# Kernel tuning notes

Hardware: AMD Instinct MI355X
Metric: run time of the kernel (lower is better)

Reference implementation:

```python
import jax, jax.numpy as jnp
import numpy as np

DIM = 512; D_STATE = 8; D_CONV = 3; EXPAND = 1; WIN = 7; N = WIN * WIN
D_INNER = EXPAND * DIM; D_HALF = D_INNER // 2
DT_RANK = -(-DIM // 16)  # 32
E = DT_RANK + 2 * D_STATE  # 48
B_WIN = 512


def _diag_flat(w):
    idx = []
    for s in range(2 * w - 1):
        for r in range(max(0, s - (w - 1)), min(w - 1, s) + 1):
            idx.append(r * w + (s - r))
    return np.array(idx, dtype=np.int32)


def _anti_flat(w):
    idx = []
    for s in range(2 * w - 1):
        for r in range(max(0, s - (w - 1)), min(w - 1, s) + 1):
            c = s - r
            idx.append(r * w + (w - 1 - c))
    return np.array(idx, dtype=np.int32)

DIAG_IDX = jnp.asarray(_diag_flat(WIN))
ANTI_IDX = jnp.asarray(_anti_flat(WIN))
V_IDX = jnp.asarray(np.arange(N).reshape(WIN, WIN).T.reshape(-1).astype(np.int32))


def setup_inputs() -> dict:
    key = jax.random.key(0)
    ks = iter(jax.random.split(key, 32))
    f32 = jnp.float32
    def lin_w(k, out_d, in_d):
        return (jax.random.normal(k, (out_d, in_d), f32) * (in_d ** -0.5)).astype(f32)
    inp = {}
    inp['tokens'] = jax.random.normal(next(ks), (B_WIN, N, DIM), f32)
    for nm in ['pre_h', 'pre_v', 'pre_d', 'pre_a', 'post_h', 'post_v', 'post_d', 'post_a']:
        inp[nm + '_w'] = lin_w(next(ks), DIM, DIM)
        inp[nm + '_b'] = jnp.zeros((DIM,), f32)
    inp['in_proj_w'] = lin_w(next(ks), D_INNER, DIM)
    inp['conv_x_w'] = jax.random.normal(next(ks), (D_HALF, 1, D_CONV), f32) * (D_CONV ** -0.5)
    inp['conv_x_b'] = jnp.zeros((D_HALF,), f32)
    inp['conv_z_w'] = jax.random.normal(next(ks), (D_HALF, 1, D_CONV), f32) * (D_CONV ** -0.5)
    inp['conv_z_b'] = jnp.zeros((D_HALF,), f32)
    inp['x_proj_w'] = lin_w(next(ks), E, D_HALF)
    inp['ln_w'] = jnp.ones((E,), f32)
    inp['ln_b'] = jnp.zeros((E,), f32)
    dt_std = DT_RANK ** -0.5
    inp['dt_proj_w'] = jax.random.uniform(next(ks), (D_HALF, DT_RANK), f32, -dt_std, dt_std)
    u = jax.random.uniform(next(ks), (D_HALF,), f32)
    dt = jnp.clip(jnp.exp(u * (np.log(0.1) - np.log(0.001)) + np.log(0.001)), 1e-4, None)
    inp['dt_proj_b'] = dt + jnp.log(-jnp.expm1(-dt))
    inp['A_log'] = jnp.tile(jnp.log(jnp.arange(1, D_STATE + 1, dtype=f32))[None, :], (D_HALF, 1))
    inp['D_param'] = jnp.ones((D_HALF,), f32)
    inp['out_proj_w'] = lin_w(next(ks), DIM, D_INNER)
    inp['gate_logits'] = jnp.zeros((4,), f32)
    return inp


def _linear(x, W, b=None):
    y = x @ W.T
    return y if b is None else y + b


def _dwconv_same(x, w, b):
    # x: (b, d, l), w: (d, 1, k) depthwise, cross-correlation like torch
    y = jax.lax.conv_general_dilated(x, w, window_strides=(1,), padding='SAME',
                                     dimension_numbers=('NCH', 'OIH', 'NCH'),
                                     feature_group_count=x.shape[1])
    return y + b[None, :, None]


def _layernorm(x, g, b, eps=1e-5):
    m = jnp.mean(x, -1, keepdims=True)
    v = jnp.var(x, -1, keepdims=True)
    return (x - m) * jax.lax.rsqrt(v + eps) * g + b


def _selective_scan(u, delta, A, Bm, Cm, D, delta_bias):
    # u, delta: (b,d,l); A: (d,n); Bm, Cm: (b,n,l); D: (d,)
    delta = jax.nn.softplus(delta + delta_bias[None, :, None])
    u_l = jnp.moveaxis(u, 2, 0)       # (l,b,d)
    d_l = jnp.moveaxis(delta, 2, 0)   # (l,b,d)
    B_l = jnp.moveaxis(Bm, 2, 0)      # (l,b,n)
    C_l = jnp.moveaxis(Cm, 2, 0)      # (l,b,n)
    h0 = jnp.zeros((u.shape[0], u.shape[1], A.shape[1]), u.dtype)  # (b,d,n)

    def step(h, t):
        dt_t, u_t, B_t, C_t = t
        dA = jnp.exp(dt_t[:, :, None] * A[None])          # (b,d,n)
        dBu = dt_t[:, :, None] * B_t[:, None, :] * u_t[:, :, None]
        h = h * dA + dBu
        y = jnp.einsum('bdn,bn->bd', h, C_t)
        return h, y

    _, ys = jax.lax.scan(step, h0, (d_l, u_l, B_l, C_l))
    y = jnp.moveaxis(ys, 0, 2)  # (b,d,l)
    return y + D[None, :, None] * u


def _mamba_core(x_seq, p):
    b, L, _ = x_seq.shape
    xz = _linear(x_seq, p['in_proj_w'])              # (b,l,d_inner)
    xz = jnp.swapaxes(xz, 1, 2)                      # (b,d_inner,l)
    x, z = jnp.split(xz, 2, axis=1)                  # each (b,d_half,l)
    x_conv = jax.nn.silu(_dwconv_same(x, p['conv_x_w'], p['conv_x_b']))
    z_conv = jax.nn.silu(_dwconv_same(z, p['conv_z_w'], p['conv_z_b']))
    A = -jnp.exp(p['A_log'])
    x_dbl = jnp.einsum('bdl,ed->ble', x_conv, p['x_proj_w'])  # (b,l,E)
    x_dbl = _layernorm(x_dbl, p['ln_w'], p['ln_b'])
    dt, Bm, Cm = jnp.split(x_dbl, [DT_RANK, DT_RANK + D_STATE], axis=-1)
    dt = jnp.swapaxes(_linear(dt, p['dt_proj_w']), 1, 2)      # (b,d_half,l)
    Bm = jnp.swapaxes(Bm, 1, 2)                                # (b,n,l)
    Cm = jnp.swapaxes(Cm, 1, 2)
    y = _selective_scan(x_conv, dt, A, Bm, Cm, p['D_param'], p['dt_proj_b'])
    y = jnp.nan_to_num(y)
    y = jnp.concatenate([y, z_conv], axis=1)                   # (b,d_inner,l)
    y = jnp.swapaxes(y, 1, 2)
    return _linear(y, p['out_proj_w'])


def reference(tokens, pre_h_w, pre_h_b, pre_v_w, pre_v_b, pre_d_w, pre_d_b,
              pre_a_w, pre_a_b, in_proj_w, conv_x_w, conv_x_b, conv_z_w, conv_z_b,
              x_proj_w, ln_w, ln_b, dt_proj_w, dt_proj_b, A_log, D_param,
              out_proj_w, post_h_w, post_h_b, post_v_w, post_v_b, post_d_w,
              post_d_b, post_a_w, post_a_b, gate_logits):
    p = dict(in_proj_w=in_proj_w, conv_x_w=conv_x_w, conv_x_b=conv_x_b,
             conv_z_w=conv_z_w, conv_z_b=conv_z_b, x_proj_w=x_proj_w,
             ln_w=ln_w, ln_b=ln_b, dt_proj_w=dt_proj_w, dt_proj_b=dt_proj_b,
             A_log=A_log, D_param=D_param, out_proj_w=out_proj_w)
    rh = _linear(tokens, pre_h_w, pre_h_b)
    rv = _linear(tokens, pre_v_w, pre_v_b)[:, V_IDX, :]
    rd = _linear(tokens, pre_d_w, pre_d_b)[:, DIAG_IDX, :]
    ra = _linear(tokens, pre_a_w, pre_a_b)[:, ANTI_IDX, :]
    r_all = jnp.concatenate([rh, rv, rd, ra], axis=0)
    y_all = _mamba_core(r_all, p)
    yh, yv, yd, ya = jnp.split(y_all, 4, axis=0)
    yh = _linear(yh, post_h_w, post_h_b)
    yv = _linear(yv, post_v_w, post_v_b)
    yd = _linear(yd, post_d_w, post_d_b)
    ya = _linear(ya, post_a_w, post_a_b)
    g = jax.nn.softmax(gate_logits)
    return g[0] * yh + g[1] * yv + g[2] * yd + g[3] * ya
```

## Files before the change

kernel.cpp:

```cpp
#include <hip/hip_runtime.h>
#include <stdint.h>

typedef __attribute__((ext_vector_type(8))) short bf16x8;
typedef __attribute__((ext_vector_type(4))) float f32x4;

__device__ __forceinline__ float bf2f(short u){
  union { float f; uint32_t i; } v; v.i = ((uint32_t)(uint16_t)u) << 16; return v.f;
}
__device__ __forceinline__ short f2bf(float x){
  union { float f; uint32_t i; } v; v.f = x;
  uint32_t r = v.i + 0x7FFFu + ((v.i >> 16) & 1u);
  return (short)(r >> 16);
}

__device__ __forceinline__ void gl_lds16(const short* g, short* l){
  __builtin_amdgcn_global_load_lds(
      (__attribute__((address_space(1))) void*)(short*)g,
      (__attribute__((address_space(3))) void*)l, 16, 0, 0);
}

__device__ const int d_DIAG[49] = {0,1,7,2,8,14,3,9,15,21,4,10,16,22,28,5,11,17,23,29,35,
  6,12,18,24,30,36,42,13,19,25,31,37,43,20,26,32,38,44,27,33,39,45,34,40,46,41,47,48};
__device__ const int d_ANTI[49] = {6,5,13,4,12,20,3,11,19,27,2,10,18,26,34,1,9,17,25,33,41,
  0,8,16,24,32,40,48,7,15,23,31,39,47,14,22,30,38,46,21,29,37,45,28,36,44,35,43,42};

__device__ __forceinline__ int perm_idx(int g, int l){
  if (g == 0) return l;
  if (g == 1) return (l % 7) * 7 + l / 7;
  if (g == 2) return d_DIAG[l];
  return d_ANTI[l];
}

template<int NT>
__device__ __forceinline__ void kcore256x128(
    const short* aU0, const short* aU1, const short* bU,
    short* S, int w, int lane, f32x4 acc[4][4])
{
  int wr = w >> 1, wc = w & 1;
  int mr = lane & 15, quad = lane >> 4;
  int sw = (quad ^ ((mr >> 1) & 3)) * 8;
  auto STAGE_A = [&](int t){
    short* base = S + (t & 1) * 12288;
    gl_lds16(aU0 + t*32, base + (w*32)*32);
    gl_lds16(aU1 + t*32, base + (w*32 + 16)*32);
  };
  auto STAGE_B = [&](int t){
    short* base = S + (t & 1) * 12288;
    gl_lds16(bU + t*32, base + 8192 + (w*16)*32);
  };
  STAGE_A(0); STAGE_B(0);
  if (NT > 1) STAGE_A(1);
  asm volatile("s_waitcnt vmcnt(2)" ::: "memory");
  __builtin_amdgcn_s_barrier();
  for (int t = 0; t < NT; ++t){
    const short* Ab = S + (t & 1) * 12288;
    const short* Bb = Ab + 8192;
    bf16x8 bfr[4];
    #pragma unroll
    for (int nf = 0; nf < 4; ++nf)
      bfr[nf] = *(const bf16x8*)(Bb + (wc*64 + nf*16 + mr)*32 + sw);
    #pragma unroll
    for (int ph = 0; ph < 4; ++ph){
      bf16x8 af = *(const bf16x8*)(Ab + (wr*64 + ph*16 + mr)*32 + sw);
      if (ph == 1 && t+1 < NT) STAGE_B(t+1);
      #pragma unroll
      for (int nf = 0; nf < 4; ++nf)
        acc[ph][nf] = __builtin_amdgcn_mfma_f32_16x16x32_bf16(af, bfr[nf], acc[ph][nf],0,0,0);
    }
    __builtin_amdgcn_s_barrier();
    if (t+2 < NT){
      STAGE_A(t+2);
      asm volatile("s_waitcnt vmcnt(2)" ::: "memory");
    } else if (t+1 < NT){
      asm volatile("s_waitcnt vmcnt(0)" ::: "memory");
    }
    __builtin_amdgcn_s_barrier();
  }
}

__global__ __launch_bounds__(256) void k_conv_all(
    const float* __restrict__ in_proj,
    const float* __restrict__ pw0, const float* __restrict__ pw1,
    const float* __restrict__ pw2, const float* __restrict__ pw3,
    const float* __restrict__ xpw, const float* __restrict__ dtw,
    short* __restrict__ inp_bf, short* __restrict__ postw_bf,
    short* __restrict__ xpw_bf, short* __restrict__ dtw_bf)
{
  int q = blockIdx.x*256 + threadIdx.x;
  const float* src; short* dst; int off;
  if (q < 65536){ src = in_proj; dst = inp_bf; off = q; }
  else if (q < 65536 + 262144){
    int r = q - 65536; int g = r >> 16; int loc = r & 65535;
    src = (g==0)?pw0:(g==1)?pw1:(g==2)?pw2:pw3;
    dst = postw_bf + g*262144; off = loc;
  }
  else if (q < 65536 + 262144 + 3072){ src = xpw; dst = xpw_bf; off = q - (65536+262144); }
  else { src = dtw; dst = dtw_bf; off = q - (65536+262144+3072); }
  float4 v = *(const float4*)(src + off*4);
  uint32_t p0 = (uint32_t)(uint16_t)f2bf(v.x) | ((uint32_t)(uint16_t)f2bf(v.y) << 16);
  uint32_t p1 = (uint32_t)(uint16_t)f2bf(v.z) | ((uint32_t)(uint16_t)f2bf(v.w) << 16);
  uint2 p; p.x = p0; p.y = p1;
  *(uint2*)(dst + off*4) = p;
}

__global__ __launch_bounds__(256) void k_transp(
    const float* __restrict__ pw0, const float* __restrict__ pw1,
    const float* __restrict__ pw2, const float* __restrict__ pw3,
    const float* __restrict__ outp,
    short* __restrict__ wpreT, short* __restrict__ woutT)
{
  __shared__ float tile[64][65];
  int which = blockIdx.y;
  const float* src = (which==0)?pw0:(which==1)?pw1:(which==2)?pw2:(which==3)?pw3:outp;
  short* dst = (which < 4) ? (wpreT + which*262144) : woutT;
  int bi = blockIdx.x >> 3, bj = blockIdx.x & 7;
  int r0 = bi*64, c0 = bj*64;
  int t = threadIdx.x;
  int row = t >> 2, cg = t & 3;
  const float4* s4 = (const float4*)(src + (r0+row)*512 + c0 + cg*16);
  #pragma unroll
  for (int i=0;i<4;i++){
    float4 v = s4[i];
    tile[row][cg*16 + i*4 + 0] = v.x;
    tile[row][cg*16 + i*4 + 1] = v.y;
    tile[row][cg*16 + i*4 + 2] = v.z;
    tile[row][cg*16 + i*4 + 3] = v.w;
  }
  __syncthreads();
  int oc = t >> 2;
  short tmp[16];
  #pragma unroll
  for (int i=0;i<16;i++) tmp[i] = f2bf(tile[cg*16 + i][oc]);
  short* dp = dst + (size_t)(c0+oc)*512 + r0 + cg*16;
  *(bf16x8*)(dp)     = *(bf16x8*)tmp;
  *(bf16x8*)(dp + 8) = *((bf16x8*)tmp + 1);
}

__global__ __launch_bounds__(256) void k_tok(const float* __restrict__ t, short* __restrict__ o){
  int i = (blockIdx.x*256 + threadIdx.x) * 4;
  float4 v = *(const float4*)(t + i);
  uint32_t p0 = (uint32_t)(uint16_t)f2bf(v.x) | ((uint32_t)(uint16_t)f2bf(v.y) << 16);
  uint32_t p1 = (uint32_t)(uint16_t)f2bf(v.z) | ((uint32_t)(uint16_t)f2bf(v.w) << 16);
  uint2 p; p.x = p0; p.y = p1;
  *(uint2*)(o + i) = p;
}

__global__ __launch_bounds__(256) void k_bxz_gains(const float* __restrict__ in_proj,
    const float* __restrict__ b0, const float* __restrict__ b1,
    const float* __restrict__ b2, const float* __restrict__ b3,
    const float* __restrict__ gl,
    const float* __restrict__ pb0, const float* __restrict__ pb1,
    const float* __restrict__ pb2, const float* __restrict__ pb3,
    float* __restrict__ bxz, float* __restrict__ gains, float* __restrict__ biasc)
{
  if (blockIdx.x < 8){
    int idx = blockIdx.x*256 + threadIdx.x;
    int g = idx >> 9, i = idx & 511;
    const float* bb = (g==0)?b0:(g==1)?b1:(g==2)?b2:b3;
    float s = 0.f;
    for (int t=0;t<512;t++) s += in_proj[i*512+t]*bb[t];
    bxz[idx] = s;
  } else {
    float m = fmaxf(fmaxf(gl[0], gl[1]), fmaxf(gl[2], gl[3]));
    float e0 = expf(gl[0]-m), e1 = expf(gl[1]-m), e2 = expf(gl[2]-m), e3 = expf(gl[3]-m);
    float s = e0+e1+e2+e3;
    float g0 = e0/s, g1 = e1/s, g2 = e2/s, g3 = e3/s;
    int t = threadIdx.x;
    if (t == 0){ gains[0]=g0; gains[1]=g1; gains[2]=g2; gains[3]=g3; }
    biasc[t]     = g0*pb0[t]     + g1*pb1[t]     + g2*pb2[t]     + g3*pb3[t];
    biasc[t+256] = g0*pb0[t+256] + g1*pb1[t+256] + g2*pb2[t+256] + g3*pb3[t+256];
  }
}

__device__ __forceinline__ void mfma_2x4_k(const short* a0, const short* a1,
    const short* b0, const short* b1, const short* b2, const short* b3,
    int K, f32x4 acc[2][4])
{
  for (int k0 = 0; k0 < K; k0 += 32){
    bf16x8 av0 = *(const bf16x8*)(a0 + k0);
    bf16x8 av1 = *(const bf16x8*)(a1 + k0);
    bf16x8 bv0 = *(const bf16x8*)(b0 + k0);
    bf16x8 bv1 = *(const bf16x8*)(b1 + k0);
    bf16x8 bv2 = *(const bf16x8*)(b2 + k0);
    bf16x8 bv3 = *(const bf16x8*)(b3 + k0);
    acc[0][0] = __builtin_amdgcn_mfma_f32_16x16x32_bf16(av0, bv0, acc[0][0],0,0,0);
    acc[0][1] = __builtin_amdgcn_mfma_f32_16x16x32_bf16(av0, bv1, acc[0][1],0,0,0);
    acc[0][2] = __builtin_amdgcn_mfma_f32_16x16x32_bf16(av0, bv2, acc[0][2],0,0,0);
    acc[0][3] = __builtin_amdgcn_mfma_f32_16x16x32_bf16(av0, bv3, acc[0][3],0,0,0);
    acc[1][0] = __builtin_amdgcn_mfma_f32_16x16x32_bf16(av1, bv0, acc[1][0],0,0,0);
    acc[1][1] = __builtin_amdgcn_mfma_f32_16x16x32_bf16(av1, bv1, acc[1][1],0,0,0);
    acc[1][2] = __builtin_amdgcn_mfma_f32_16x16x32_bf16(av1, bv2, acc[1][2],0,0,0);
    acc[1][3] = __builtin_amdgcn_mfma_f32_16x16x32_bf16(av1, bv3, acc[1][3],0,0,0);
  }
}

__global__ __launch_bounds__(256) void k_wfuse(const short* __restrict__ inp_bf,
    const short* __restrict__ wpreT, const short* __restrict__ postw_bf,
    const short* __restrict__ woutT, const float* __restrict__ gains,
    short* __restrict__ wxz, short* __restrict__ wogc)
{
  int z = blockIdx.z; int g = z & 3, which = z >> 2;
  int bn = blockIdx.x * 64, bm = blockIdx.y * 128;
  int lane = threadIdx.x & 63, wave = threadIdx.x >> 6;
  int mr = lane & 15, qk = (lane >> 4) * 8, quad = lane >> 4;
  const short* Am = which ? (postw_bf + g*262144) : inp_bf;
  const short* Bm = which ? woutT : (wpreT + g*262144);
  const short* a0 = Am + (bm + wave*32 + mr)*512 + qk;
  const short* a1 = a0 + 16*512;
  const short* b0 = Bm + (bn +  0 + mr)*512 + qk;
  const short* b1 = Bm + (bn + 16 + mr)*512 + qk;
  const short* b2 = Bm + (bn + 32 + mr)*512 + qk;
  const short* b3 = Bm + (bn + 48 + mr)*512 + qk;
  f32x4 acc[2][4] = {};
  mfma_2x4_k(a0, a1, b0, b1, b2, b3, 512, acc);
  float gain = which ? gains[g] : 1.f;
  #pragma unroll
  for (int s=0;s<2;s++)
    #pragma unroll
    for (int t=0;t<4;t++)
      #pragma unroll
      for (int r=0;r<4;r++){
        int row = bm + wave*32 + s*16 + quad*4 + r;
        int col = bn + t*16 + mr;
        if (which) wogc[row*2048 + g*512 + col] = f2bf(gain * acc[s][t][r]);
        else       wxz[g*262144 + row*512 + col] = f2bf(acc[s][t][r]);
      }
}

__global__ __launch_bounds__(512) void k_gemm1c(const short* __restrict__ tok,
    const short* __restrict__ wxz, const float* __restrict__ bxz,
    const float* __restrict__ cxw, const float* __restrict__ cxb,
    const float* __restrict__ czw, const float* __restrict__ czb,
    short* __restrict__ ycat)
{
  __shared__ __align__(16) short S[24576];
  int bid = blockIdx.x;
  int swz = (bid & 7) * 206 + (bid >> 3);
  int g = swz / 412, rem = swz - g*412;
  int blk = rem >> 2, bn = (rem & 3) * 128;
  int bm = blk * 245;
  int nreal = min(245, 25088 - bm);
  int tid = threadIdx.x, lane = tid & 63, w = tid >> 6;

  int rl = lane >> 2;
  int gch = ((lane & 3) ^ ((lane >> 3) & 3)) * 8;
  const short* aU[2];
  #pragma unroll
  for (int j = 0; j < 2; ++j){
    int p = w*32 + j*16 + rl;
    int pr = (p < nreal) ? p : (nreal - 1);
    int q49 = pr / 49;
    int l49 = pr - q49*49;
    int b = blk*5 + q49;
    int sl = perm_idx(g, l49);
    aU[j] = tok + ((size_t)(b*49 + sl))*512 + gch;
  }
  const short* bU = wxz + (size_t)g*262144 + (size_t)(bn + w*16 + rl)*512 + gch;

  f32x4 acc[4][4] = {};
  kcore256x128<16>(aU[0], aU[1], bU, S, w, lane, acc);

  int wr = w >> 1, wc = w & 1, mr = lane & 15, quad = lane >> 4;
  int rowgrp = tid >> 3, oct = tid & 7;
  #pragma unroll
  for (int h = 0; h < 2; ++h){
    if (wc == h){
      #pragma unroll
      for (int mf = 0; mf < 4; ++mf)
        #pragma unroll
        for (int nf = 0; nf < 4; ++nf)
          #pragma unroll
          for (int rr = 0; rr < 4; ++rr){
            int row = wr*64 + mf*16 + quad*4 + rr;
            int col = nf*16 + mr;
            S[row*72 + col] = f2bf(acc[mf][nf][rr] + bxz[g*512 + bn + h*64 + col]);
          }
    }
    __syncthreads();
    int colbase = bn + h*64 + oct*8;
    bool isx = colbase < 256;
    const float* wsrc = isx ? cxw : czw;
    const float* bsrc = isx ? cxb : czb;
    int cc0 = isx ? colbase : colbase - 256;
    float w0[8], w1[8], w2[8], cb[8];
    #pragma unroll
    for (int e = 0; e < 8; ++e){
      w0[e] = wsrc[(cc0+e)*3]; w1[e] = wsrc[(cc0+e)*3+1]; w2[e] = wsrc[(cc0+e)*3+2];
      cb[e] = bsrc[cc0+e];
    }
    for (int i = 0; i < 4; ++i){
      int p = rowgrp + 64*i;
      if (p < nreal){
        int l = p - (p/49)*49;
        bf16x8 vm = {}, vp = {};
        bf16x8 v0 = *(const bf16x8*)(S + p*72 + oct*8);
        if (l > 0)  vm = *(const bf16x8*)(S + (p-1)*72 + oct*8);
        if (l < 48) vp = *(const bf16x8*)(S + (p+1)*72 + oct*8);
        short ov[8];
        #pragma unroll
        for (int e = 0; e < 8; ++e){
          float x = w0[e]*bf2f(vm[e]) + w1[e]*bf2f(v0[e]) + w2[e]*bf2f(vp[e]) + cb[e];
          ov[e] = f2bf(x / (1.f + __expf(-x)));
        }
        *(bf16x8*)(ycat + (size_t)(bm + p)*2048 + g*512 + colbase) = *(bf16x8*)ov;
      }
    }
    __syncthreads();
  }
}

__global__ __launch_bounds__(256) void k_xproj(const short* __restrict__ ycat,
    const short* __restrict__ xpw_bf, const float* __restrict__ lnw, const float* __restrict__ lnb,
    const short* __restrict__ dtw_bf, const float* __restrict__ dtb,
    short* __restrict__ dtln, float* __restrict__ bc)
{
  __shared__ __align__(16) char smem[36864];
  float* xd = (float*)smem;
  short* xln = (short*)(smem + 26624);

  int bm = blockIdx.x * 128;
  int g = bm / 25088;
  int tid = threadIdx.x, lane = tid & 63, w = tid >> 6;
  int mr = lane & 15, quad = lane >> 4, qk = quad * 8;

  {
    const short* ap[2];
    #pragma unroll
    for (int s=0;s<2;s++)
      ap[s] = ycat + (size_t)(bm - g*25088 + w*32 + s*16 + mr)*2048 + g*512 + qk;
    f32x4 acc[2][3] = {};
    #pragma unroll
    for (int k0 = 0; k0 < 256; k0 += 32){
      bf16x8 av[2];
      #pragma unroll
      for (int s=0;s<2;s++) av[s] = *(const bf16x8*)(ap[s] + k0);
      #pragma unroll
      for (int t=0;t<3;t++){
        bf16x8 bv = *(const bf16x8*)(xpw_bf + (t*16 + mr)*256 + qk + k0);
        #pragma unroll
        for (int s=0;s<2;s++)
          acc[s][t] = __builtin_amdgcn_mfma_f32_16x16x32_bf16(av[s], bv, acc[s][t],0,0,0);
      }
    }
    #pragma unroll
    for (int s=0;s<2;s++)
      #pragma unroll
      for (int t=0;t<3;t++)
        #pragma unroll
        for (int r=0;r<4;r++)
          xd[(w*32 + s*16 + quad*4 + r)*52 + t*16 + mr] = acc[s][t][r];
  }
  __syncthreads();

  if (tid < 128){
    f32x4* xr4 = (f32x4*)(xd + tid*52);
    f32x4 s = xr4[0];
    #pragma unroll
    for (int i=1;i<12;i++) s += xr4[i];
    float m = (s[0]+s[1]+s[2]+s[3]) * (1.f/48.f);
    f32x4 vs = {};
    #pragma unroll
    for (int i=0;i<12;i++){ f32x4 d = xr4[i] - m; vs += d*d; }
    float var = (vs[0]+vs[1]+vs[2]+vs[3]) * (1.f/48.f);
    float rstd = rsqrtf(var + 1e-5f);
    const f32x4* g4 = (const f32x4*)lnw;
    const f32x4* b4 = (const f32x4*)lnb;
    uint32_t* xlr = (uint32_t*)(xln + tid*40);
    #pragma unroll
    for (int i=0;i<8;i++){
      f32x4 v = (xr4[i] - m) * rstd * g4[i] + b4[i];
      xlr[2*i]   = (uint32_t)(uint16_t)f2bf(v[0]) | ((uint32_t)(uint16_t)f2bf(v[1]) << 16);
      xlr[2*i+1] = (uint32_t)(uint16_t)f2bf(v[2]) | ((uint32_t)(uint16_t)f2bf(v[3]) << 16);
    }
    f32x4* bco = (f32x4*)(bc + (size_t)(bm + tid)*16);
    #pragma unroll
    for (int i=8;i<12;i++)
      bco[i-8] = (xr4[i] - m) * rstd * g4[i] + b4[i];
  }
  __syncthreads();

  {
    bf16x8 a[2];
    #pragma unroll
    for (int s=0;s<2;s++)
      a[s] = *(const bf16x8*)(xln + (w*32 + s*16 + mr)*40 + qk);
    #pragma unroll 4
    for (int nt=0; nt<16; nt++){
      int col = nt*16 + mr;
      bf16x8 bv = *(const bf16x8*)(dtw_bf + col*32 + qk);
      float dtbv = dtb[col];
      #pragma unroll
      for (int s=0;s<2;s++){
        f32x4 acc = {};
        acc = __builtin_amdgcn_mfma_f32_16x16x32_bf16(a[s], bv, acc,0,0,0);
        #pragma unroll
        for (int r=0;r<4;r++){
          int grow = bm + w*32 + s*16 + quad*4 + r;
          float dtv = acc[r] + dtbv;
          float e  = __expf(dtv);
          float sp = __logf(1.f + e);
          float delta = (dtv > 15.f) ? dtv : sp;
          dtln[(size_t)grow*256 + col] = f2bf(delta);
        }
      }
    }
  }
}

__global__ __launch_bounds__(256) void k_scan(short* __restrict__ ycat,
    const short* __restrict__ dtln, const float* __restrict__ bc,
    const float* __restrict__ Alog, const float* __restrict__ Dp)
{
  __shared__ __align__(16) float bcs[784];
  int gb = blockIdx.x; int g = gb >> 9, b = gb & 511;
  int d = threadIdx.x;
  if (d < 196) ((f32x4*)bcs)[d] = ((const f32x4*)(bc + (size_t)gb*784))[d];
  __syncthreads();

  float A[8], h[8];
  {
    f32x4 a0 = *(const f32x4*)(Alog + d*8);
    f32x4 a1 = *(const f32x4*)(Alog + d*8 + 4);
    #pragma unroll
    for (int n=0;n<4;n++){ A[n] = -__expf(a0[n]); A[n+4] = -__expf(a1[n]); h[n]=0.f; h[n+4]=0.f; }
  }
  float Dpar = Dp[d];

  const short* dptr = dtln + (size_t)gb*49*256 + d;
  short* uptr = ycat + (size_t)(b*49)*2048 + g*512 + d;

  float dn = bf2f(dptr[0]);
  float un = bf2f(uptr[0]);
  for (int l=0;l<49;l++){
    float delta = dn, u = un;
    if (l < 48){ dn = bf2f(dptr[(l+1)*256]); un = bf2f(uptr[(l+1)*2048]); }
    const f32x4* bcr = (const f32x4*)(bcs + l*16);
    f32x4 B0 = bcr[0], B1 = bcr[1], C0 = bcr[2], C1 = bcr[3];
    float du = delta * u;
    float y = 0.f;
    #pragma unroll
    for (int n=0;n<4;n++){
      h[n] = h[n]*__expf(delta*A[n]) + du*B0[n];
      y += h[n]*C0[n];
    }
    #pragma unroll
    for (int n=0;n<4;n++){
      h[n+4] = h[n+4]*__expf(delta*A[n+4]) + du*B1[n];
      y += h[n+4]*C1[n];
    }
    uptr[l*2048] = f2bf(y + Dpar*u);
  }
}

__global__ __launch_bounds__(512) void k_gemmF(const short* __restrict__ ycat,
    const short* __restrict__ wogc, const float* __restrict__ biasc,
    float* __restrict__ out)
{
  __shared__ __align__(16) short S[24576];
  int bid = blockIdx.x;
  int swz = (bid & 7) * 49 + (bid >> 3);
  int bm = (swz >> 2) * 256, bn = (swz & 3) * 128;
  int tid = threadIdx.x, lane = tid & 63, w = tid >> 6;

  int rl = lane >> 2;
  int gch = ((lane & 3) ^ ((lane >> 3) & 3)) * 8;
  const short* aU0 = ycat + (size_t)(bm + w*32      + rl)*2048 + gch;
  const short* aU1 = ycat + (size_t)(bm + w*32 + 16 + rl)*2048 + gch;
  const short* bU  = wogc + (size_t)(bn + w*16      + rl)*2048 + gch;

  f32x4 acc[4][4] = {};
  kcore256x128<64>(aU0, aU1, bU, S, w, lane, acc);

  int wr = w >> 1, wc = w & 1, mr = lane & 15, quad = lane >> 4;
  #pragma unroll
  for (int mf = 0; mf < 4; ++mf)
    #pragma unroll
    for (int rr = 0; rr < 4; ++rr){
      int row = bm + wr*64 + mf*16 + quad*4 + rr;
      float* orow = out + (size_t)row*512;
      #pragma unroll
      for (int nf = 0; nf < 4; ++nf){
        int col = bn + wc*64 + nf*16 + mr;
        orow[col] = acc[mf][nf][rr] + biasc[col];
      }
    }
}

extern "C" void kernel_launch(void* const* d_in, const int* in_sizes, int n_in,
                              void* d_out, int out_size, void* d_ws, size_t ws_size,
                              hipStream_t stream)
{
  const float* tokens    = (const float*)d_in[0];
  const float* pre_w[4]  = {(const float*)d_in[1], (const float*)d_in[3], (const float*)d_in[5], (const float*)d_in[7]};
  const float* pre_b[4]  = {(const float*)d_in[2], (const float*)d_in[4], (const float*)d_in[6], (const float*)d_in[8]};
  const float* post_w[4] = {(const float*)d_in[9], (const float*)d_in[11], (const float*)d_in[13], (const float*)d_in[15]};
  const float* post_b[4] = {(const float*)d_in[10], (const float*)d_in[12], (const float*)d_in[14], (const float*)d_in[16]};
  const float* in_proj   = (const float*)d_in[17];
  const float* conv_x_w  = (const float*)d_in[18];
  const float* conv_x_b  = (const float*)d_in[19];
  const float* conv_z_w  = (const float*)d_in[20];
  const float* conv_z_b  = (const float*)d_in[21];
  const float* x_proj_w  = (const float*)d_in[22];
  const float* ln_w      = (const float*)d_in[23];
  const float* ln_b      = (const float*)d_in[24];
  const float* dt_proj_w = (const float*)d_in[25];
  const float* dt_proj_b = (const float*)d_in[26];
  const float* A_log     = (const float*)d_in[27];
  const float* D_param   = (const float*)d_in[28];
  const float* out_proj  = (const float*)d_in[29];
  const float* gate_log  = (const float*)d_in[30];

  char* ws = (char*)d_ws;
  size_t o = 0;
  short* tok_bf   = (short*)(ws + o); o += 25690112;
  short* wpreT    = (short*)(ws + o); o += 2097152;
  short* inp_bf   = (short*)(ws + o); o += 524288;
  short* postw_bf = (short*)(ws + o); o += 2097152;
  short* woutT    = (short*)(ws + o); o += 524288;
  short* wogc     = (short*)(ws + o); o += 2097152;
  short* wxz      = (short*)(ws + o); o += 2097152;
  short* xpw_bf   = (short*)(ws + o); o += 24576;
  short* dtw_bf   = (short*)(ws + o); o += 16384;
  float* bxz      = (float*)(ws + o); o += 8192;
  float* gains    = (float*)(ws + o); o += 64;
  float* biasc    = (float*)(ws + o); o += 2048;
  size_t scratch_off = o;
  o += 102760448;
  short* ycat     = (short*)(ws + o); o += 102760448;
  short* dtln     = (short*)(ws + scratch_off);
  float* bc       = (float*)(ws + scratch_off + 51380224);

  k_conv_all<<<1300, 256, 0, stream>>>(in_proj,
      post_w[0], post_w[1], post_w[2], post_w[3],
      x_proj_w, dt_proj_w, inp_bf, postw_bf, xpw_bf, dtw_bf);
  k_transp<<<dim3(64,5), 256, 0, stream>>>(pre_w[0], pre_w[1], pre_w[2], pre_w[3],
      out_proj, wpreT, woutT);
  k_tok<<<12544, 256, 0, stream>>>(tokens, tok_bf);
  k_bxz_gains<<<9, 256, 0, stream>>>(in_proj, pre_b[0], pre_b[1], pre_b[2], pre_b[3],
      gate_log, post_b[0], post_b[1], post_b[2], post_b[3], bxz, gains, biasc);
  k_wfuse<<<dim3(8,4,8), 256, 0, stream>>>(inp_bf, wpreT, postw_bf, woutT, gains, wxz, wogc);
  k_gemm1c<<<dim3(1648), 512, 0, stream>>>(tok_bf, wxz, bxz,
      conv_x_w, conv_x_b, conv_z_w, conv_z_b, ycat);
  k_xproj<<<784, 256, 0, stream>>>(ycat, xpw_bf, ln_w, ln_b, dtw_bf, dt_proj_b, dtln, bc);
  k_scan<<<2048, 256, 0, stream>>>(ycat, dtln, bc, A_log, D_param);
  k_gemmF<<<dim3(392), 512, 0, stream>>>(ycat, wogc, biasc, (float*)d_out);
}
```

Baseline: 453.1 us.

## Fuse x-projection, layernorm, dt projection and selective scan into one kernel

Merges the x_proj/LN/dt_proj kernel with the selective scan kernel so each block handles one (group, window) sequence of 49 tokens. The u tile, delta and B/C values stay in LDS instead of going through global scratch buffers, which removes the dtln/bc write and read traffic and one kernel launch. In exchange, the MFMA tiles are padded from 49 to 64 rows, which wastes some compute, and the larger LDS footprint of about 58KB per block may reduce occupancy. A block-index swizzle is also added.

```diff
diff --git a/kernel.cpp b/kernel.cpp
--- a/kernel.cpp
+++ b/kernel.cpp
@@ -309,50 +309,55 @@
   }
 }
 
-__global__ __launch_bounds__(256) void k_xproj(const short* __restrict__ ycat,
+__global__ __launch_bounds__(256) void k_xps(short* __restrict__ ycat,
     const short* __restrict__ xpw_bf, const float* __restrict__ lnw, const float* __restrict__ lnb,
     const short* __restrict__ dtw_bf, const float* __restrict__ dtb,
-    short* __restrict__ dtln, float* __restrict__ bc)
-{
-  __shared__ __align__(16) char smem[36864];
-  float* xd = (float*)smem;
-  short* xln = (short*)(smem + 26624);
-
-  int bm = blockIdx.x * 128;
-  int g = bm / 25088;
+    const float* __restrict__ Alog, const float* __restrict__ Dp)
+{
+  __shared__ __align__(16) char smem[58016];
+  short* Us  = (short*)smem;
+  short* xln = (short*)(smem + 25872);
+  float* bcs = (float*)(smem + 29792);
+  float* xd  = (float*)(smem + 32928);
+  short* ddt = (short*)(smem + 32928);
+
+  int bid = blockIdx.x;
+  int swz = (bid & 7) * 256 + (bid >> 3);
+  int g = swz >> 9, b = swz & 511;
   int tid = threadIdx.x, lane = tid & 63, w = tid >> 6;
   int mr = lane & 15, quad = lane >> 4, qk = quad * 8;
 
+  const short* ubase = ycat + (size_t)(b*49)*2048 + g*512;
+  for (int idx = tid; idx < 1568; idx += 256){
+    int l = idx >> 5, cc = (idx & 31) * 8;
+    *(bf16x8*)(Us + l*264 + cc) = *(const bf16x8*)(ubase + (size_t)l*2048 + cc);
+  }
+  __syncthreads();
+
   {
-    const short* ap[2];
-    #pragma unroll
-    for (int s=0;s<2;s++)
-      ap[s] = ycat + (size_t)(bm - g*25088 + w*32 + s*16 + mr)*2048 + g*512 + qk;
-    f32x4 acc[2][3] = {};
+    int ar = w*16 + mr; if (ar > 48) ar = 48;
+    const short* ap = Us + ar*264 + qk;
+    f32x4 acc[3] = {};
     #pragma unroll
     for (int k0 = 0; k0 < 256; k0 += 32){
-      bf16x8 av[2];
-      #pragma unroll
-      for (int s=0;s<2;s++) av[s] = *(const bf16x8*)(ap[s] + k0);
-      #pragma unroll
-      for (int t=0;t<3;t++){
+      bf16x8 av = *(const bf16x8*)(ap + k0);
+      #pragma unroll
+      for (int t = 0; t < 3; ++t){
         bf16x8 bv = *(const bf16x8*)(xpw_bf + (t*16 + mr)*256 + qk + k0);
-        #pragma unroll
-        for (int s=0;s<2;s++)
-          acc[s][t] = __builtin_amdgcn_mfma_f32_16x16x32_bf16(av[s], bv, acc[s][t],0,0,0);
-      }
-    }
-    #pragma unroll
-    for (int s=0;s<2;s++)
-      #pragma unroll
-      for (int t=0;t<3;t++)
-        #pragma unroll
-        for (int r=0;r<4;r++)
-          xd[(w*32 + s*16 + quad*4 + r)*52 + t*16 + mr] = acc[s][t][r];
+        acc[t] = __builtin_amdgcn_mfma_f32_16x16x32_bf16(av, bv, acc[t],0,0,0);
+      }
+    }
+    #pragma unroll
+    for (int t = 0; t < 3; ++t)
+      #pragma unroll
+      for (int r = 0; r < 4; ++r){
+        int row = w*16 + quad*4 + r;
+        if (row < 49) xd[row*52 + t*16 + mr] = acc[t][r];
+      }
   }
   __syncthreads();
 
-  if (tid < 128){
+  if (tid < 49){
     f32x4* xr4 = (f32x4*)(xd + tid*52);
     f32x4 s = xr4[0];
     #pragma unroll
@@ -372,7 +377,7 @@
       xlr[2*i]   = (uint32_t)(uint16_t)f2bf(v[0]) | ((uint32_t)(uint16_t)f2bf(v[1]) << 16);
       xlr[2*i+1] = (uint32_t)(uint16_t)f2bf(v[2]) | ((uint32_t)(uint16_t)f2bf(v[3]) << 16);
     }
-    f32x4* bco = (f32x4*)(bc + (size_t)(bm + tid)*16);
+    f32x4* bco = (f32x4*)(bcs + tid*16);
     #pragma unroll
     for (int i=8;i<12;i++)
       bco[i-8] = (xr4[i] - m) * rstd * g4[i] + b4[i];
@@ -380,75 +385,59 @@
   __syncthreads();
 
   {
-    bf16x8 a[2];
-    #pragma unroll
-    for (int s=0;s<2;s++)
-      a[s] = *(const bf16x8*)(xln + (w*32 + s*16 + mr)*40 + qk);
+    int ar = w*16 + mr; if (ar > 48) ar = 48;
+    bf16x8 a = *(const bf16x8*)(xln + ar*40 + qk);
     #pragma unroll 4
     for (int nt=0; nt<16; nt++){
       int col = nt*16 + mr;
       bf16x8 bv = *(const bf16x8*)(dtw_bf + col*32 + qk);
       float dtbv = dtb[col];
-      #pragma unroll
-      for (int s=0;s<2;s++){
-        f32x4 acc = {};
-        acc = __builtin_amdgcn_mfma_f32_16x16x32_bf16(a[s], bv, acc,0,0,0);
-        #pragma unroll
-        for (int r=0;r<4;r++){
-          int grow = bm + w*32 + s*16 + quad*4 + r;
+      f32x4 acc = {};
+      acc = __builtin_amdgcn_mfma_f32_16x16x32_bf16(a, bv, acc,0,0,0);
+      #pragma unroll
+      for (int r=0;r<4;r++){
+        int row = w*16 + quad*4 + r;
+        if (row < 49){
           float dtv = acc[r] + dtbv;
           float e  = __expf(dtv);
           float sp = __logf(1.f + e);
           float delta = (dtv > 15.f) ? dtv : sp;
-          dtln[(size_t)grow*256 + col] = f2bf(delta);
+          ddt[row*256 + col] = f2bf(delta);
         }
       }
     }
   }
-}
-
-__global__ __launch_bounds__(256) void k_scan(short* __restrict__ ycat,
-    const short* __restrict__ dtln, const float* __restrict__ bc,
-    const float* __restrict__ Alog, const float* __restrict__ Dp)
-{
-  __shared__ __align__(16) float bcs[784];
-  int gb = blockIdx.x; int g = gb >> 9, b = gb & 511;
-  int d = threadIdx.x;
-  if (d < 196) ((f32x4*)bcs)[d] = ((const f32x4*)(bc + (size_t)gb*784))[d];
   __syncthreads();
 
-  float A[8], h[8];
   {
+    int d = tid;
+    float A[8], h[8];
     f32x4 a0 = *(const f32x4*)(Alog + d*8);
     f32x4 a1 = *(const f32x4*)(Alog + d*8 + 4);
     #pragma unroll
     for (int n=0;n<4;n++){ A[n] = -__expf(a0[n]); A[n+4] = -__expf(a1[n]); h[n]=0.f; h[n+4]=0.f; }
-  }
-  float Dpar = Dp[d];
-
-  const short* dptr = dtln + (size_t)gb*49*256 + d;
-  short* uptr = ycat + (size_t)(b*49)*2048 + g*512 + d;
-
-  float dn = bf2f(dptr[0]);
-  float un = bf2f(uptr[0]);
-  for (int l=0;l<49;l++){
-    float delta = dn, u = un;
-    if (l < 48){ dn = bf2f(dptr[(l+1)*256]); un = bf2f(uptr[(l+1)*2048]); }
-    const f32x4* bcr = (const f32x4*)(bcs + l*16);
-    f32x4 B0 = bcr[0], B1 = bcr[1], C0 = bcr[2], C1 = bcr[3];
-    float du = delta * u;
-    float y = 0.f;
-    #pragma unroll
-    for (int n=0;n<4;n++){
-      h[n] = h[n]*__expf(delta*A[n]) + du*B0[n];
-      y += h[n]*C0[n];
-    }
-    #pragma unroll
-    for (int n=0;n<4;n++){
-      h[n+4] = h[n+4]*__expf(delta*A[n+4]) + du*B1[n];
-      y += h[n+4]*C1[n];
-    }
-    uptr[l*2048] = f2bf(y + Dpar*u);
+    float Dpar = Dp[d];
+    short* uptr = ycat + (size_t)(b*49)*2048 + g*512 + d;
+
+    for (int l=0;l<49;l++){
+      float delta = bf2f(ddt[l*256 + d]);
+      float u     = bf2f(Us[l*264 + d]);
+      const f32x4* bcr = (const f32x4*)(bcs + l*16);
+      f32x4 B0 = bcr[0], B1 = bcr[1], C0 = bcr[2], C1 = bcr[3];
+      float du = delta * u;
+      float y = 0.f;
+      #pragma unroll
+      for (int n=0;n<4;n++){
+        h[n] = h[n]*__expf(delta*A[n]) + du*B0[n];
+        y += h[n]*C0[n];
+      }
+      #pragma unroll
+      for (int n=0;n<4;n++){
+        h[n+4] = h[n+4]*__expf(delta*A[n+4]) + du*B1[n];
+        y += h[n+4]*C1[n];
+      }
+      uptr[l*2048] = f2bf(y + Dpar*u);
+    }
   }
 }
 
@@ -527,8 +516,7 @@
   size_t scratch_off = o;
   o += 102760448;
   short* ycat     = (short*)(ws + o); o += 102760448;
-  short* dtln     = (short*)(ws + scratch_off);
-  float* bc       = (float*)(ws + scratch_off + 51380224);
+  (void)scratch_off;
 
   k_conv_all<<<1300, 256, 0, stream>>>(in_proj,
       post_w[0], post_w[1], post_w[2], post_w[3],
@@ -541,7 +529,7 @@
   k_wfuse<<<dim3(8,4,8), 256, 0, stream>>>(inp_bf, wpreT, postw_bf, woutT, gains, wxz, wogc);
   k_gemm1c<<<dim3(1648), 512, 0, stream>>>(tok_bf, wxz, bxz,
       conv_x_w, conv_x_b, conv_z_w, conv_z_b, ycat);
-  k_xproj<<<784, 256, 0, stream>>>(ycat, xpw_bf, ln_w, ln_b, dtw_bf, dt_proj_b, dtln, bc);
-  k_scan<<<2048, 256, 0, stream>>>(ycat, dtln, bc, A_log, D_param);
+  k_xps<<<dim3(2048), 256, 0, stream>>>(ycat, xpw_bf, ln_w, ln_b,
+      dtw_bf, dt_proj_b, A_log, D_param);
   k_gemmF<<<dim3(392), 512, 0, stream>>>(ycat, wogc, biasc, (float*)d_out);
 }
```

Result: no change. 459.6 us (+1.4%).
